# Optimization experiments

Measured on AMD Instinct MI355X. Metric: run time of the kernel, lower is better.

Reference implementation:

```python
import jax, jax.numpy as jnp
import numpy as np

N_NODES = 100000
N_EDGES = 1600000
NUM_GRAPHS = 256


def _gcn_conv(x, src, dst, deg_isqrt, deg_inv, W, b):
    # GCNConv with self-loops and symmetric normalization (PyG semantics):
    # out_i = sum_{j->i} d_j^-1/2 d_i^-1/2 (x_j W) + d_i^-1 (x_i W) + b
    xl = x @ W  # [N, out]
    norm = deg_isqrt[src] * deg_isqrt[dst]  # [E]
    msgs = norm[:, None] * xl[src]  # [E, out] -- dominant memory traffic
    agg = jax.ops.segment_sum(msgs, dst, num_segments=N_NODES)
    return agg + deg_inv[:, None] * xl + b


def setup_inputs() -> dict:
    key = jax.random.key(0)
    ks = jax.random.split(key, 8)
    F_in, H, T = 128, 128, 64
    x = jax.random.normal(ks[0], (N_NODES, F_in), dtype=jnp.float32)
    edge_index = jax.random.randint(ks[1], (2, N_EDGES), 0, N_NODES, dtype=jnp.int64)
    batch = jnp.sort(jax.random.randint(ks[2], (N_NODES,), 0, NUM_GRAPHS, dtype=jnp.int64))
    s0 = 1.0 / np.sqrt(F_in)
    s1 = 1.0 / np.sqrt(H)
    return {
        "x": x,
        "edge_index": edge_index,
        "batch": batch,
        "W0": jax.random.normal(ks[3], (F_in, H), dtype=jnp.float32) * s0,
        "b0": jnp.zeros((H,), dtype=jnp.float32),
        "W1": jax.random.normal(ks[4], (H, H), dtype=jnp.float32) * s1,
        "b1": jnp.zeros((H,), dtype=jnp.float32),
        "W2": jax.random.normal(ks[5], (H, T), dtype=jnp.float32) * s1,
        "b2": jnp.zeros((T,), dtype=jnp.float32),
    }


def reference(x, edge_index, batch, W0, b0, W1, b1, W2, b2):
    src, dst = edge_index[0], edge_index[1]
    # degree including self-loop
    deg = jax.ops.segment_sum(jnp.ones((N_EDGES,), x.dtype), dst, num_segments=N_NODES) + 1.0
    deg_isqrt = jax.lax.rsqrt(deg)
    deg_inv = 1.0 / deg

    h = jax.nn.gelu(_gcn_conv(x, src, dst, deg_isqrt, deg_inv, W0, b0))
    h = jax.nn.gelu(_gcn_conv(h, src, dst, deg_isqrt, deg_inv, W1, b1))
    h = jax.nn.gelu(_gcn_conv(h, src, dst, deg_isqrt, deg_inv, W2, b2))

    # global_mean_pool over graphs
    sums = jax.ops.segment_sum(h, batch, num_segments=NUM_GRAPHS)
    counts = jax.ops.segment_sum(jnp.ones((N_NODES,), h.dtype), batch, num_segments=NUM_GRAPHS)
    return sums / jnp.maximum(counts, 1.0)[:, None]
```

## Files before the change

kernel.cpp:

```cpp
#include <hip/hip_runtime.h>
#include <math.h>

#define F_IN 128
#define TDIM 64
#define NGRAPH 256

typedef __attribute__((ext_vector_type(8))) short short8;
typedef __attribute__((ext_vector_type(4))) float f32x4;

__device__ __forceinline__ float gelu_f(float x) {
    float x3 = x * x * x;
    return 0.5f * x * (1.0f + tanhf(0.7978845608028654f * (x + 0.044715f * x3)));
}

__device__ __forceinline__ unsigned short bf16_of(float x) {
    unsigned u = __float_as_uint(x);
    return (unsigned short)((u + 0x7fffu + ((u >> 16) & 1u)) >> 16);
}
__device__ __forceinline__ float f_of(unsigned short h) {
    return __uint_as_float(((unsigned)h) << 16);
}
__device__ __forceinline__ unsigned bf16pair(float a, float b) {
    return (unsigned)bf16_of(a) | ((unsigned)bf16_of(b) << 16);
}
__device__ __forceinline__ float2 bf16unpack(unsigned u) {
    float2 r;
    r.x = __uint_as_float(u << 16);
    r.y = __uint_as_float(u & 0xffff0000u);
    return r;
}


#define BIN_CH 4096
#define MAXNB 512
#define CAP 6144

__global__ __launch_bounds__(256) void binC_kernel(const int* __restrict__ src,
                                                   const int* __restrict__ dst,
                                                   int* __restrict__ bucket_cnt,
                                                   unsigned* __restrict__ tmp, int E, int NB) {
    __shared__ int hist[MAXNB];
    __shared__ int hbase[MAXNB];
    __shared__ int hcur[MAXNB];
    int tid = threadIdx.x;
    int base = blockIdx.x * BIN_CH;
    int end = base + BIN_CH;
    if (end > E) end = E;
    for (int i = tid; i < NB; i += 256) hist[i] = 0;
    __syncthreads();
    for (int e = base + tid; e < end; e += 256) atomicAdd(&hist[dst[e] >> 8], 1);
    __syncthreads();
    for (int i = tid; i < NB; i += 256) {
        int c = hist[i];
        hbase[i] = (c > 0) ? atomicAdd(&bucket_cnt[i], c) : 0;
        hcur[i] = 0;
    }
    __syncthreads();
    for (int e = base + tid; e < end; e += 256) {
        int d = dst[e];
        int b = d >> 8;
        int p = atomicAdd(&hcur[b], 1);
        int slot = hbase[b] + p;
        if (slot < CAP)
            tmp[(size_t)b * CAP + slot] = (unsigned)src[e] | ((unsigned)(d & 255) << 24);
    }
}

__global__ __launch_bounds__(256) void scan_wconv_kernel(const int* __restrict__ bucket_cnt,
                                                         int* __restrict__ bbase,
                                                         int* __restrict__ row_off, int NB,
                                                         int N, const float* __restrict__ W0,
                                                         const float* __restrict__ W1,
                                                         const float* __restrict__ W2,
                                                         unsigned short* __restrict__ hi0,
                                                         unsigned short* __restrict__ lo0,
                                                         unsigned short* __restrict__ hi1,
                                                         unsigned short* __restrict__ lo1,
                                                         unsigned short* __restrict__ hi2,
                                                         unsigned short* __restrict__ lo2) {
    if (blockIdx.x == 0) {
        if (threadIdx.x == 0) {
            int c = 0;
            for (int i = 0; i < NB; ++i) {
                bbase[i] = c;
                int v = bucket_cnt[i];
                c += (v < CAP ? v : CAP);
            }
            row_off[N] = c;
        }
        return;
    }
    int idx = (blockIdx.x - 1) * 256 + threadIdx.x;
    const float* W;
    unsigned short *whi, *wlo;
    int local, FOUT;
    if (idx < 16384) {
        W = W0; whi = hi0; wlo = lo0; local = idx; FOUT = 128;
    } else if (idx < 32768) {
        W = W1; whi = hi1; wlo = lo1; local = idx - 16384; FOUT = 128;
    } else if (idx < 40960) {
        W = W2; whi = hi2; wlo = lo2; local = idx - 32768; FOUT = 64;
    } else {
        return;
    }
    int k = local / FOUT;
    int n = local % FOUT;
    float w = W[local];
    unsigned short h = bf16_of(w);
    whi[(size_t)n * 128 + k] = h;
    wlo[(size_t)n * 128 + k] = bf16_of(w - f_of(h));
}

__global__ __launch_bounds__(256) void binDcount_kernel(const unsigned* __restrict__ tmp,
                                                        const int* __restrict__ bucket_cnt,
                                                        const int* __restrict__ bbase,
                                                        int* __restrict__ row_off,
                                                        float* __restrict__ isq,
                                                        float* __restrict__ dinv, int N) {
    __shared__ int lcnt[256];
    __shared__ int sh[256];
    int b = blockIdx.x;
    int tid = threadIdx.x;
    int cntb = bucket_cnt[b];
    if (cntb > CAP) cntb = CAP;
    lcnt[tid] = 0;
    __syncthreads();
    const unsigned* tb = tmp + (size_t)b * CAP;
    for (int e = tid; e < cntb; e += 256) atomicAdd(&lcnt[tb[e] >> 24], 1);
    __syncthreads();
    int own = lcnt[tid];
    sh[tid] = own;
    __syncthreads();
    for (int off = 1; off < 256; off <<= 1) {
        int x = (tid >= off) ? sh[tid - off] : 0;
        __syncthreads();
        sh[tid] += x;
        __syncthreads();
    }
    int excl = sh[tid] - own;
    int node = (b << 8) + tid;
    if (node < N) {
        row_off[node] = bbase[b] + excl;
        float d = (float)own + 1.0f;
        isq[node] = rsqrtf(d);
        dinv[node] = 1.0f / d;
    }
}

__global__ __launch_bounds__(256) void binDscatter_kernel(const unsigned* __restrict__ tmp,
                                                          const int* __restrict__ bucket_cnt,
                                                          const int* __restrict__ row_off,
                                                          const float* __restrict__ isq,
                                                          uint2* __restrict__ edges, int N) {
    __shared__ int lcur[256];
    __shared__ float lisq[256];
    int b = blockIdx.x;
    int node0 = b << 8;
    int tid = threadIdx.x;
    lcur[tid] = 0;
    int nd = node0 + tid;
    lisq[tid] = (nd < N) ? isq[nd] : 0.f;
    __syncthreads();
    int cntb = bucket_cnt[b];
    if (cntb > CAP) cntb = CAP;
    const unsigned* tb = tmp + (size_t)b * CAP;
    for (int e = tid; e < cntb; e += 256) {
        unsigned rec = tb[e];
        int dl = (int)(rec >> 24);
        unsigned s = rec & 0xFFFFFFu;
        int p = atomicAdd(&lcur[dl], 1);
        float nrm = isq[s] * lisq[dl];
        edges[(size_t)row_off[node0 + dl] + p] = make_uint2(s, __float_as_uint(nrm));
    }
}


#define LROW 136

__global__ __launch_bounds__(256) void gemm_f32_kernel(const float* __restrict__ X,
                                                       const unsigned short* __restrict__ whiT,
                                                       const unsigned short* __restrict__ wloT,
                                                       unsigned* __restrict__ Yb, int nrows) {
    constexpr int FOUT = 128;
    constexpr int NT = FOUT / 16;
    __shared__ short lds[2 * FOUT * LROW];
    short* shi = lds;
    short* slo = lds + FOUT * LROW;

    for (int c = threadIdx.x; c < FOUT * 16; c += 256) {
        int n = c >> 4, r = c & 15;
        *(short8*)(shi + n * LROW + r * 8) = *(const short8*)(whiT + (size_t)n * 128 + r * 8);
        *(short8*)(slo + n * LROW + r * 8) = *(const short8*)(wloT + (size_t)n * 128 + r * 8);
    }
    __syncthreads();

    int lane = threadIdx.x & 63;
    int wave = threadIdx.x >> 6;
    int quad = lane >> 4;
    int l16 = lane & 15;
    int rowBase = blockIdx.x * 128 + wave * 32;

    f32x4 acc[2][NT];
#pragma unroll
    for (int m = 0; m < 2; ++m)
#pragma unroll
        for (int t = 0; t < NT; ++t) acc[m][t] = (f32x4){0.f, 0.f, 0.f, 0.f};

    int arow0 = rowBase + l16;
    int arow1 = rowBase + 16 + l16;
    bool ok0 = arow0 < nrows, ok1 = arow1 < nrows;
    const float* xr0 = X + (size_t)arow0 * 128;
    const float* xr1 = X + (size_t)arow1 * 128;

#pragma unroll
    for (int k0 = 0; k0 < 128; k0 += 32) {
        short8 ahi[2], alo[2];
#pragma unroll
        for (int m = 0; m < 2; ++m) {
            const float* xr = m ? xr1 : xr0;
            bool ok = m ? ok1 : ok0;
            float xv[8];
            if (ok) {
                float4 v0 = *(const float4*)(xr + k0 + quad * 8);
                float4 v1 = *(const float4*)(xr + k0 + quad * 8 + 4);
                xv[0] = v0.x; xv[1] = v0.y; xv[2] = v0.z; xv[3] = v0.w;
                xv[4] = v1.x; xv[5] = v1.y; xv[6] = v1.z; xv[7] = v1.w;
            } else {
#pragma unroll
                for (int j = 0; j < 8; ++j) xv[j] = 0.f;
            }
#pragma unroll
            for (int j = 0; j < 8; ++j) {
                unsigned short h = bf16_of(xv[j]);
                ahi[m][j] = (short)h;
                alo[m][j] = (short)bf16_of(xv[j] - f_of(h));
            }
        }
#pragma unroll
        for (int t = 0; t < NT; ++t) {
            int off = (t * 16 + l16) * LROW + k0 + quad * 8;
            short8 bhi = *(const short8*)(shi + off);
            short8 blo = *(const short8*)(slo + off);
#pragma unroll
            for (int m = 0; m < 2; ++m) {
                acc[m][t] = __builtin_amdgcn_mfma_f32_16x16x32_bf16(ahi[m], bhi, acc[m][t], 0, 0, 0);
                acc[m][t] = __builtin_amdgcn_mfma_f32_16x16x32_bf16(alo[m], bhi, acc[m][t], 0, 0, 0);
                acc[m][t] = __builtin_amdgcn_mfma_f32_16x16x32_bf16(ahi[m], blo, acc[m][t], 0, 0, 0);
            }
        }
    }

#pragma unroll
    for (int m = 0; m < 2; ++m) {
#pragma unroll
        for (int t = 0; t < NT; ++t) {
            int col = t * 16 + l16;
#pragma unroll
            for (int i = 0; i < 4; ++i) {
                int r = rowBase + m * 16 + quad * 4 + i;
                float v = acc[m][t][i];
                float nb = __shfl_xor(v, 1, 64);
                if (((lane & 1) == 0) && r < nrows)
                    Yb[(size_t)r * (FOUT / 2) + (col >> 1)] = bf16pair(v, nb);
            }
        }
    }
}


template <int FOUT>
__global__ __launch_bounds__(256) void gemm_bf16_kernel(const unsigned* __restrict__ Xb,
                                                        const unsigned short* __restrict__ whiT,
                                                        const unsigned short* __restrict__ wloT,
                                                        unsigned* __restrict__ Yb, int nrows) {
    constexpr int NT = FOUT / 16;
    __shared__ short lds[2 * FOUT * LROW];
    short* shi = lds;
    short* slo = lds + FOUT * LROW;

    for (int c = threadIdx.x; c < FOUT * 16; c += 256) {
        int n = c >> 4, r = c & 15;
        *(short8*)(shi + n * LROW + r * 8) = *(const short8*)(whiT + (size_t)n * 128 + r * 8);
        *(short8*)(slo + n * LROW + r * 8) = *(const short8*)(wloT + (size_t)n * 128 + r * 8);
    }
    __syncthreads();

    int lane = threadIdx.x & 63;
    int wave = threadIdx.x >> 6;
    int quad = lane >> 4;
    int l16 = lane & 15;
    int rowBase = blockIdx.x * 128 + wave * 32;

    f32x4 acc[2][NT];
#pragma unroll
    for (int m = 0; m < 2; ++m)
#pragma unroll
        for (int t = 0; t < NT; ++t) acc[m][t] = (f32x4){0.f, 0.f, 0.f, 0.f};

    int arow0 = rowBase + l16;
    int arow1 = rowBase + 16 + l16;
    bool ok0 = arow0 < nrows, ok1 = arow1 < nrows;
    const short* xs0 = (const short*)Xb + (size_t)arow0 * 128;
    const short* xs1 = (const short*)Xb + (size_t)arow1 * 128;

#pragma unroll
    for (int k0 = 0; k0 < 128; k0 += 32) {
        short8 a[2];
#pragma unroll
        for (int m = 0; m < 2; ++m) {
            const short* xs = m ? xs1 : xs0;
            bool ok = m ? ok1 : ok0;
            if (ok)
                a[m] = *(const short8*)(xs + k0 + quad * 8);
            else
                a[m] = (short8){0, 0, 0, 0, 0, 0, 0, 0};
        }
#pragma unroll
        for (int t = 0; t < NT; ++t) {
            int off = (t * 16 + l16) * LROW + k0 + quad * 8;
            short8 bhi = *(const short8*)(shi + off);
            short8 blo = *(const short8*)(slo + off);
#pragma unroll
            for (int m = 0; m < 2; ++m) {
                acc[m][t] = __builtin_amdgcn_mfma_f32_16x16x32_bf16(a[m], bhi, acc[m][t], 0, 0, 0);
                acc[m][t] = __builtin_amdgcn_mfma_f32_16x16x32_bf16(a[m], blo, acc[m][t], 0, 0, 0);
            }
        }
    }

#pragma unroll
    for (int m = 0; m < 2; ++m) {
#pragma unroll
        for (int t = 0; t < NT; ++t) {
            int col = t * 16 + l16;
#pragma unroll
            for (int i = 0; i < 4; ++i) {
                int r = rowBase + m * 16 + quad * 4 + i;
                float v = acc[m][t][i];
                float nb = __shfl_xor(v, 1, 64);
                if (((lane & 1) == 0) && r < nrows)
                    Yb[(size_t)r * (FOUT / 2) + (col >> 1)] = bf16pair(v, nb);
            }
        }
    }
}


__global__ __launch_bounds__(256) void agg128_kernel(const unsigned* __restrict__ xlb,
                                                     const int* __restrict__ row_off,
                                                     const uint2* __restrict__ edges,
                                                     const float* __restrict__ dinv,
                                                     const float* __restrict__ bias,
                                                     unsigned* __restrict__ outb, int nnodes) {
    int wave = (blockIdx.x * blockDim.x + threadIdx.x) >> 6;
    int lane = threadIdx.x & 63;
    if (wave >= nnodes) return;
    int e0 = __builtin_amdgcn_readfirstlane(row_off[wave]);
    int e1 = __builtin_amdgcn_readfirstlane(row_off[wave + 1]);
    float ax = 0.f, ay = 0.f;
    int rounds = (e1 - e0 + 15) >> 4;
    for (int r = 0; r < rounds; ++r) {
        int base = e0 + (r << 4);
        int idx = base + (lane & 15);
        int cl = idx < e1 ? idx : e1 - 1;
        uint2 edv = edges[cl];
        unsigned sx[16];
        float nw[16];
#pragma unroll
        for (int j = 0; j < 16; ++j) {
            sx[j] = (unsigned)__builtin_amdgcn_readlane((int)edv.x, j);
            unsigned ny = (unsigned)__builtin_amdgcn_readlane((int)edv.y, j);
            nw[j] = (base + j < e1) ? __uint_as_float(ny) : 0.f;
        }
        unsigned v[16];
#pragma unroll
        for (int j = 0; j < 16; ++j) v[j] = xlb[(size_t)sx[j] * 64 + lane];
#pragma unroll
        for (int j = 0; j < 16; ++j) {
            float2 f = bf16unpack(v[j]);
            ax += nw[j] * f.x;
            ay += nw[j] * f.y;
        }
    }
    float di = dinv[wave];
    float2 pi = bf16unpack(xlb[(size_t)wave * 64 + lane]);
    float2 bb = *(const float2*)(bias + lane * 2);
    outb[(size_t)wave * 64 + lane] =
        bf16pair(gelu_f(ax + di * pi.x + bb.x), gelu_f(ay + di * pi.y + bb.y));
}


__global__ __launch_bounds__(256) void agg64_kernel(const unsigned* __restrict__ xlb,
                                                    const int* __restrict__ row_off,
                                                    const uint2* __restrict__ edges,
                                                    const float* __restrict__ dinv,
                                                    const float* __restrict__ bias,
                                                    unsigned* __restrict__ outb, int nnodes) {
    int wave = (blockIdx.x * blockDim.x + threadIdx.x) >> 6;
    int lane = threadIdx.x & 63;
    int sub = lane >> 5;
    int sl = lane & 31;
    int node = wave * 2 + sub;
    bool nv = node < nnodes;
    int e0 = nv ? row_off[node] : 0;
    int e1 = nv ? row_off[node + 1] : 0;
    int rounds = (e1 - e0 + 15) >> 4;
    int ro = __shfl_xor(rounds, 32, 64);
    int maxr = rounds > ro ? rounds : ro;
    float ax = 0.f, ay = 0.f;
    for (int r = 0; r < maxr; ++r) {
        int base = e0 + (r << 4);
        uint2 ed[16];
#pragma unroll
        for (int j = 0; j < 16; ++j) {
            int idx = base + j;
            int cl = idx < e1 ? idx : (e1 > e0 ? e1 - 1 : 0);
            ed[j] = edges[cl];
            if (idx >= e1) ed[j].y = 0u;
        }
        unsigned v[16];
#pragma unroll
        for (int j = 0; j < 16; ++j) v[j] = xlb[(size_t)ed[j].x * 32 + sl];
#pragma unroll
        for (int j = 0; j < 16; ++j) {
            float nw = __uint_as_float(ed[j].y);
            float2 f = bf16unpack(v[j]);
            ax += nw * f.x;
            ay += nw * f.y;
        }
    }
    if (nv) {
        float di = dinv[node];
        float2 pi = bf16unpack(xlb[(size_t)node * 32 + sl]);
        float2 bb = *(const float2*)(bias + sl * 2);
        outb[(size_t)node * 32 + sl] =
            bf16pair(gelu_f(ax + di * pi.x + bb.x), gelu_f(ay + di * pi.y + bb.y));
    }
}


#define POOL_CHUNK 64

__global__ __launch_bounds__(256) void pool_kernel(const unsigned* __restrict__ hb,
                                                   const int* __restrict__ batch,
                                                   float* __restrict__ psum,
                                                   float* __restrict__ pcnt, int nnodes) {
    int wave = (blockIdx.x * blockDim.x + threadIdx.x) >> 6;
    int lane = threadIdx.x & 63;
    int half = lane >> 5;
    int p = lane & 31;
    int n0 = wave * POOL_CHUNK + half * 32;
    if (n0 >= nnodes) return;
    int n1 = n0 + 32;
    if (n1 > nnodes) n1 = nnodes;

    int g_cur = batch[n0];
    float accx = 0.f, accy = 0.f;
    int cnt = 0;
    for (int node = n0; node < n1; ++node) {
        int g = batch[node];
        if (g != g_cur) {
            atomicAdd(&psum[g_cur * TDIM + 2 * p], accx);
            atomicAdd(&psum[g_cur * TDIM + 2 * p + 1], accy);
            if (p == 0) atomicAdd(&pcnt[g_cur], (float)cnt);
            accx = 0.f;
            accy = 0.f;
            cnt = 0;
            g_cur = g;
        }
        float2 f = bf16unpack(hb[(size_t)node * 32 + p]);
        accx += f.x;
        accy += f.y;
        ++cnt;
    }
    atomicAdd(&psum[g_cur * TDIM + 2 * p], accx);
    atomicAdd(&psum[g_cur * TDIM + 2 * p + 1], accy);
    if (p == 0) atomicAdd(&pcnt[g_cur], (float)cnt);
}

__global__ __launch_bounds__(256) void fin_kernel(const float* __restrict__ psum,
                                                  const float* __restrict__ pcnt,
                                                  float* __restrict__ out) {
    int i = blockIdx.x * blockDim.x + threadIdx.x;
    if (i < NGRAPH * TDIM) {
        float c = pcnt[i >> 6];
        out[i] = psum[i] / fmaxf(c, 1.0f);
    }
}


extern "C" void kernel_launch(void* const* d_in, const int* in_sizes, int n_in,
                              void* d_out, int out_size, void* d_ws, size_t ws_size,
                              hipStream_t stream) {
    const float* x = (const float*)d_in[0];
    const int* ei = (const int*)d_in[1];
    const int* batch = (const int*)d_in[2];
    const float* W0 = (const float*)d_in[3];
    const float* b0 = (const float*)d_in[4];
    const float* W1 = (const float*)d_in[5];
    const float* b1 = (const float*)d_in[6];
    const float* W2 = (const float*)d_in[7];
    const float* b2 = (const float*)d_in[8];

    const int N = in_sizes[0] / F_IN;
    const int E = in_sizes[1] / 2;
    const int* src = ei;
    const int* dst = ei + E;
    const int NB = (N + 255) >> 8;

    char* w = (char*)d_ws;
    auto alloc = [&](size_t bytes) -> void* {
        void* p = (void*)w;
        w += (bytes + 255) & ~(size_t)255;
        return p;
    };
    float* isq = (float*)alloc((size_t)N * 4);
    float* dinv = (float*)alloc((size_t)N * 4);
    int* bucket_cnt = (int*)alloc((size_t)MAXNB * 4);
    int* bbase = (int*)alloc((size_t)MAXNB * 4);
    int* row_off = (int*)alloc((size_t)(N + 1) * 4);
    uint2* edges = (uint2*)alloc((size_t)E * 8);
    unsigned* tmp = (unsigned*)alloc((size_t)NB * CAP * 4);
    float* psum = (float*)alloc((size_t)NGRAPH * TDIM * 4);
    float* pcnt = (float*)alloc((size_t)NGRAPH * 4);
    unsigned* bufXb = (unsigned*)alloc((size_t)N * 64 * 4);
    unsigned* bufHb = (unsigned*)alloc((size_t)N * 64 * 4);
    unsigned short* whiT0 = (unsigned short*)alloc(128 * 128 * 2);
    unsigned short* wloT0 = (unsigned short*)alloc(128 * 128 * 2);
    unsigned short* whiT1 = (unsigned short*)alloc(128 * 128 * 2);
    unsigned short* wloT1 = (unsigned short*)alloc(128 * 128 * 2);
    unsigned short* whiT2 = (unsigned short*)alloc(64 * 128 * 2);
    unsigned short* wloT2 = (unsigned short*)alloc(64 * 128 * 2);

    hipMemsetAsync(bucket_cnt, 0, (size_t)MAXNB * 4, stream);
    hipMemsetAsync(psum, 0, (size_t)NGRAPH * TDIM * 4, stream);
    hipMemsetAsync(pcnt, 0, (size_t)NGRAPH * 4, stream);

    int cblocks = (E + BIN_CH - 1) / BIN_CH;
    binC_kernel<<<cblocks, 256, 0, stream>>>(src, dst, bucket_cnt, tmp, E, NB);
    scan_wconv_kernel<<<1 + (40960 + 255) / 256, 256, 0, stream>>>(
        bucket_cnt, bbase, row_off, NB, N, W0, W1, W2, whiT0, wloT0, whiT1, wloT1, whiT2,
        wloT2);
    binDcount_kernel<<<NB, 256, 0, stream>>>(tmp, bucket_cnt, bbase, row_off, isq, dinv, N);
    binDscatter_kernel<<<NB, 256, 0, stream>>>(tmp, bucket_cnt, row_off, isq, edges, N);

    int gblocks = (N + 127) / 128;
    int ablocks = (N * 64 + 255) / 256;
    int a64blocks = (((N + 1) / 2) * 64 + 255) / 256;

    gemm_f32_kernel<<<gblocks, 256, 0, stream>>>(x, whiT0, wloT0, bufXb, N);
    agg128_kernel<<<ablocks, 256, 0, stream>>>(bufXb, row_off, edges, dinv, b0, bufHb, N);
    gemm_bf16_kernel<128><<<gblocks, 256, 0, stream>>>(bufHb, whiT1, wloT1, bufXb, N);
    agg128_kernel<<<ablocks, 256, 0, stream>>>(bufXb, row_off, edges, dinv, b1, bufHb, N);
    gemm_bf16_kernel<64><<<gblocks, 256, 0, stream>>>(bufHb, whiT2, wloT2, bufXb, N);
    agg64_kernel<<<a64blocks, 256, 0, stream>>>(bufXb, row_off, edges, dinv, b2, bufHb, N);

    int pwaves = (N + POOL_CHUNK - 1) / POOL_CHUNK;
    int pblocks = (pwaves * 64 + 255) / 256;
    pool_kernel<<<pblocks, 256, 0, stream>>>(bufHb, batch, psum, pcnt, N);
    fin_kernel<<<(NGRAPH * TDIM + 255) / 256, 256, 0, stream>>>(psum, pcnt, (float*)d_out);
}
```

Before: 435.8 us.

## Enlarge GEMM row tiles, drop low-bf16 weight pass, split agg tail loop

Each GEMM wave now computes 64 rows instead of 32, so every LDS weight fragment feeds four row tiles. The bf16-input GEMMs drop the low-part weight correction MFMA, halving their MFMA count and LDS footprint at some precision cost. The 128-wide aggregation loop handles full 16-edge rounds without masking and keeps a separate masked tail. Three memset calls become one small zeroing kernel.

```diff
diff --git a/kernel.cpp b/kernel.cpp
--- a/kernel.cpp
+++ b/kernel.cpp
@@ -34,6 +34,15 @@
 #define BIN_CH 4096
 #define MAXNB 512
 #define CAP 6144
+
+__global__ __launch_bounds__(256) void zero_kernel(float* __restrict__ psum,
+                                                   float* __restrict__ pcnt,
+                                                   int* __restrict__ bucket_cnt) {
+    int i = blockIdx.x * 256 + threadIdx.x;
+    if (i < NGRAPH * TDIM) psum[i] = 0.f;
+    if (i < NGRAPH) pcnt[i] = 0.f;
+    if (i < MAXNB) bucket_cnt[i] = 0;
+}
 
 __global__ __launch_bounds__(256) void binC_kernel(const int* __restrict__ src,
                                                    const int* __restrict__ dst,
@@ -198,31 +207,32 @@
     int wave = threadIdx.x >> 6;
     int quad = lane >> 4;
     int l16 = lane & 15;
-    int rowBase = blockIdx.x * 128 + wave * 32;
-
-    f32x4 acc[2][NT];
-#pragma unroll
-    for (int m = 0; m < 2; ++m)
+    int rowBase = blockIdx.x * 256 + wave * 64;
+
+    f32x4 acc[4][NT];
+#pragma unroll
+    for (int m = 0; m < 4; ++m)
 #pragma unroll
         for (int t = 0; t < NT; ++t) acc[m][t] = (f32x4){0.f, 0.f, 0.f, 0.f};
 
-    int arow0 = rowBase + l16;
-    int arow1 = rowBase + 16 + l16;
-    bool ok0 = arow0 < nrows, ok1 = arow1 < nrows;
-    const float* xr0 = X + (size_t)arow0 * 128;
-    const float* xr1 = X + (size_t)arow1 * 128;
+    const float* xr[4];
+    bool ok[4];
+#pragma unroll
+    for (int m = 0; m < 4; ++m) {
+        int arow = rowBase + m * 16 + l16;
+        ok[m] = arow < nrows;
+        xr[m] = X + (size_t)arow * 128;
+    }
 
 #pragma unroll
     for (int k0 = 0; k0 < 128; k0 += 32) {
-        short8 ahi[2], alo[2];
-#pragma unroll
-        for (int m = 0; m < 2; ++m) {
-            const float* xr = m ? xr1 : xr0;
-            bool ok = m ? ok1 : ok0;
+        short8 ahi[4], alo[4];
+#pragma unroll
+        for (int m = 0; m < 4; ++m) {
             float xv[8];
-            if (ok) {
-                float4 v0 = *(const float4*)(xr + k0 + quad * 8);
-                float4 v1 = *(const float4*)(xr + k0 + quad * 8 + 4);
+            if (ok[m]) {
+                float4 v0 = *(const float4*)(xr[m] + k0 + quad * 8);
+                float4 v1 = *(const float4*)(xr[m] + k0 + quad * 8 + 4);
                 xv[0] = v0.x; xv[1] = v0.y; xv[2] = v0.z; xv[3] = v0.w;
                 xv[4] = v1.x; xv[5] = v1.y; xv[6] = v1.z; xv[7] = v1.w;
             } else {
@@ -242,7 +252,7 @@
             short8 bhi = *(const short8*)(shi + off);
             short8 blo = *(const short8*)(slo + off);
 #pragma unroll
-            for (int m = 0; m < 2; ++m) {
+            for (int m = 0; m < 4; ++m) {
                 acc[m][t] = __builtin_amdgcn_mfma_f32_16x16x32_bf16(ahi[m], bhi, acc[m][t], 0, 0, 0);
                 acc[m][t] = __builtin_amdgcn_mfma_f32_16x16x32_bf16(alo[m], bhi, acc[m][t], 0, 0, 0);
                 acc[m][t] = __builtin_amdgcn_mfma_f32_16x16x32_bf16(ahi[m], blo, acc[m][t], 0, 0, 0);
@@ -251,7 +261,7 @@
     }
 
 #pragma unroll
-    for (int m = 0; m < 2; ++m) {
+    for (int m = 0; m < 4; ++m) {
 #pragma unroll
         for (int t = 0; t < NT; ++t) {
             int col = t * 16 + l16;
@@ -271,17 +281,13 @@
 template <int FOUT>
 __global__ __launch_bounds__(256) void gemm_bf16_kernel(const unsigned* __restrict__ Xb,
                                                         const unsigned short* __restrict__ whiT,
-                                                        const unsigned short* __restrict__ wloT,
                                                         unsigned* __restrict__ Yb, int nrows) {
     constexpr int NT = FOUT / 16;
-    __shared__ short lds[2 * FOUT * LROW];
-    short* shi = lds;
-    short* slo = lds + FOUT * LROW;
+    __shared__ short shi[FOUT * LROW];
 
     for (int c = threadIdx.x; c < FOUT * 16; c += 256) {
         int n = c >> 4, r = c & 15;
         *(short8*)(shi + n * LROW + r * 8) = *(const short8*)(whiT + (size_t)n * 128 + r * 8);
-        *(short8*)(slo + n * LROW + r * 8) = *(const short8*)(wloT + (size_t)n * 128 + r * 8);
     }
     __syncthreads();
 
@@ -289,47 +295,44 @@
     int wave = threadIdx.x >> 6;
     int quad = lane >> 4;
     int l16 = lane & 15;
-    int rowBase = blockIdx.x * 128 + wave * 32;
-
-    f32x4 acc[2][NT];
-#pragma unroll
-    for (int m = 0; m < 2; ++m)
+    int rowBase = blockIdx.x * 256 + wave * 64;
+
+    f32x4 acc[4][NT];
+#pragma unroll
+    for (int m = 0; m < 4; ++m)
 #pragma unroll
         for (int t = 0; t < NT; ++t) acc[m][t] = (f32x4){0.f, 0.f, 0.f, 0.f};
 
-    int arow0 = rowBase + l16;
-    int arow1 = rowBase + 16 + l16;
-    bool ok0 = arow0 < nrows, ok1 = arow1 < nrows;
-    const short* xs0 = (const short*)Xb + (size_t)arow0 * 128;
-    const short* xs1 = (const short*)Xb + (size_t)arow1 * 128;
+    const short* xs[4];
+    bool ok[4];
+#pragma unroll
+    for (int m = 0; m < 4; ++m) {
+        int arow = rowBase + m * 16 + l16;
+        ok[m] = arow < nrows;
+        xs[m] = (const short*)Xb + (size_t)arow * 128;
+    }
 
 #pragma unroll
     for (int k0 = 0; k0 < 128; k0 += 32) {
-        short8 a[2];
-#pragma unroll
-        for (int m = 0; m < 2; ++m) {
-            const short* xs = m ? xs1 : xs0;
-            bool ok = m ? ok1 : ok0;
-            if (ok)
-                a[m] = *(const short8*)(xs + k0 + quad * 8);
+        short8 a[4];
+#pragma unroll
+        for (int m = 0; m < 4; ++m) {
+            if (ok[m])
+                a[m] = *(const short8*)(xs[m] + k0 + quad * 8);
             else
                 a[m] = (short8){0, 0, 0, 0, 0, 0, 0, 0};
         }
 #pragma unroll
         for (int t = 0; t < NT; ++t) {
-            int off = (t * 16 + l16) * LROW + k0 + quad * 8;
-            short8 bhi = *(const short8*)(shi + off);
-            short8 blo = *(const short8*)(slo + off);
-#pragma unroll
-            for (int m = 0; m < 2; ++m) {
-                acc[m][t] = __builtin_amdgcn_mfma_f32_16x16x32_bf16(a[m], bhi, acc[m][t], 0, 0, 0);
-                acc[m][t] = __builtin_amdgcn_mfma_f32_16x16x32_bf16(a[m], blo, acc[m][t], 0, 0, 0);
-            }
-        }
-    }
-
-#pragma unroll
-    for (int m = 0; m < 2; ++m) {
+            short8 b = *(const short8*)(shi + (t * 16 + l16) * LROW + k0 + quad * 8);
+#pragma unroll
+            for (int m = 0; m < 4; ++m)
+                acc[m][t] = __builtin_amdgcn_mfma_f32_16x16x32_bf16(a[m], b, acc[m][t], 0, 0, 0);
+        }
+    }
+
+#pragma unroll
+    for (int m = 0; m < 4; ++m) {
 #pragma unroll
         for (int t = 0; t < NT; ++t) {
             int col = t * 16 + l16;
@@ -358,10 +361,29 @@
     int e0 = __builtin_amdgcn_readfirstlane(row_off[wave]);
     int e1 = __builtin_amdgcn_readfirstlane(row_off[wave + 1]);
     float ax = 0.f, ay = 0.f;
-    int rounds = (e1 - e0 + 15) >> 4;
-    for (int r = 0; r < rounds; ++r) {
-        int base = e0 + (r << 4);
-        int idx = base + (lane & 15);
+    int e = e0;
+    int nfull = (e1 - e0) >> 4;
+    for (int r = 0; r < nfull; ++r, e += 16) {
+        uint2 edv = edges[e + (lane & 15)];
+        unsigned sx[16];
+        float nw[16];
+#pragma unroll
+        for (int j = 0; j < 16; ++j) {
+            sx[j] = (unsigned)__builtin_amdgcn_readlane((int)edv.x, j);
+            nw[j] = __uint_as_float((unsigned)__builtin_amdgcn_readlane((int)edv.y, j));
+        }
+        unsigned v[16];
+#pragma unroll
+        for (int j = 0; j < 16; ++j) v[j] = xlb[(size_t)sx[j] * 64 + lane];
+#pragma unroll
+        for (int j = 0; j < 16; ++j) {
+            float2 f = bf16unpack(v[j]);
+            ax += nw[j] * f.x;
+            ay += nw[j] * f.y;
+        }
+    }
+    if (e < e1) {
+        int idx = e + (lane & 15);
         int cl = idx < e1 ? idx : e1 - 1;
         uint2 edv = edges[cl];
         unsigned sx[16];
@@ -370,7 +392,7 @@
         for (int j = 0; j < 16; ++j) {
             sx[j] = (unsigned)__builtin_amdgcn_readlane((int)edv.x, j);
             unsigned ny = (unsigned)__builtin_amdgcn_readlane((int)edv.y, j);
-            nw[j] = (base + j < e1) ? __uint_as_float(ny) : 0.f;
+            nw[j] = (e + j < e1) ? __uint_as_float(ny) : 0.f;
         }
         unsigned v[16];
 #pragma unroll
@@ -532,9 +554,7 @@
     unsigned short* whiT2 = (unsigned short*)alloc(64 * 128 * 2);
     unsigned short* wloT2 = (unsigned short*)alloc(64 * 128 * 2);
 
-    hipMemsetAsync(bucket_cnt, 0, (size_t)MAXNB * 4, stream);
-    hipMemsetAsync(psum, 0, (size_t)NGRAPH * TDIM * 4, stream);
-    hipMemsetAsync(pcnt, 0, (size_t)NGRAPH * 4, stream);
+    zero_kernel<<<(NGRAPH * TDIM + 255) / 256, 256, 0, stream>>>(psum, pcnt, bucket_cnt);
 
     int cblocks = (E + BIN_CH - 1) / BIN_CH;
     binC_kernel<<<cblocks, 256, 0, stream>>>(src, dst, bucket_cnt, tmp, E, NB);
@@ -544,15 +564,15 @@
     binDcount_kernel<<<NB, 256, 0, stream>>>(tmp, bucket_cnt, bbase, row_off, isq, dinv, N);
     binDscatter_kernel<<<NB, 256, 0, stream>>>(tmp, bucket_cnt, row_off, isq, edges, N);
 
-    int gblocks = (N + 127) / 128;
+    int gblocks = (N + 255) / 256;
     int ablocks = (N * 64 + 255) / 256;
     int a64blocks = (((N + 1) / 2) * 64 + 255) / 256;
 
     gemm_f32_kernel<<<gblocks, 256, 0, stream>>>(x, whiT0, wloT0, bufXb, N);
     agg128_kernel<<<ablocks, 256, 0, stream>>>(bufXb, row_off, edges, dinv, b0, bufHb, N);
-    gemm_bf16_kernel<128><<<gblocks, 256, 0, stream>>>(bufHb, whiT1, wloT1, bufXb, N);
+    gemm_bf16_kernel<128><<<gblocks, 256, 0, stream>>>(bufHb, whiT1, bufXb, N);
     agg128_kernel<<<ablocks, 256, 0, stream>>>(bufXb, row_off, edges, dinv, b1, bufHb, N);
-    gemm_bf16_kernel<64><<<gblocks, 256, 0, stream>>>(bufHb, whiT2, wloT2, bufXb, N);
+    gemm_bf16_kernel<64><<<gblocks, 256, 0, stream>>>(bufHb, whiT2, bufXb, N);
     agg64_kernel<<<a64blocks, 256, 0, stream>>>(bufXb, row_off, edges, dinv, b2, bufHb, N);
 
     int pwaves = (N + POOL_CHUNK - 1) / POOL_CHUNK;
```

Result: no change. 431.8 us (-0.9%).
